# Performance work log

Hardware: AMD Instinct MI355X
Metric: run time of the kernel (lower is better)

The kernel has to match this reference:

```python
import jax, jax.numpy as jnp
import numpy as np

N = 65536
IN_FEAT = 512
OUT_FEAT = 512
K = 16


def setup_inputs() -> dict:
    key = jax.random.key(0)
    k_feat, k_wt, k_wp, k_idx = jax.random.split(key, 4)
    feat = jax.random.normal(k_feat, (N, IN_FEAT), dtype=jnp.float32)
    # nn.Linear(in, out, bias=False): y = x @ W.T with W [out, in].
    # We store W as [in, out] so y = x @ W (same math, transposed layout).
    scale = 1.0 / np.sqrt(IN_FEAT)
    W_theta = jax.random.uniform(k_wt, (IN_FEAT, OUT_FEAT), dtype=jnp.float32, minval=-scale, maxval=scale)
    W_phi = jax.random.uniform(k_wp, (IN_FEAT, OUT_FEAT), dtype=jnp.float32, minval=-scale, maxval=scale)
    src_ind = jax.random.randint(k_idx, (N, K), 0, N, dtype=jnp.int64)
    return {"k": K, "src_ind": src_ind, "feat": feat, "W_theta": W_theta, "W_phi": W_phi}


def reference(k, src_ind, feat, W_theta, W_phi):
    # Dense projections (cuBLAS-friendly part)
    h_theta = feat @ W_theta            # [N, out]
    h_phi = feat @ W_phi                # [N, out]
    h_src = h_theta                     # message contribution from source node
    h_dst = h_phi - h_theta             # per-destination additive term
    # fused_edgeconv_op: result[i] = max_{j in 0..k} (h_src[src_ind[i, j]] + h_dst[i]).
    # h_dst[i] is constant over neighbors, so max commutes with the add:
    neigh = h_src[src_ind[:, :k]]       # [N, k, out] irregular gather
    result = jnp.max(neigh, axis=1) + h_dst  # [N, out]
    return result
```

## Files before the change

kernel.cpp:

```cpp
#include <hip/hip_runtime.h>
#include <hip/hip_bf16.h>
#include <stdint.h>


typedef __bf16 bf16x8 __attribute__((ext_vector_type(8)));
typedef float f32x4 __attribute__((ext_vector_type(4)));

__device__ __forceinline__ unsigned short f2bf(float x) {
    unsigned u = __float_as_uint(x);
    unsigned r = u + 0x7fffu + ((u >> 16) & 1u);
    return (unsigned short)(r >> 16);
}
__device__ __forceinline__ float bf2f(unsigned short b) {
    return __uint_as_float(((unsigned)b) << 16);
}

__device__ __forceinline__ void async_ld16(const void* g, void* l) {
    __builtin_amdgcn_global_load_lds(
        (const __attribute__((address_space(1))) unsigned int*)g,
        (__attribute__((address_space(3))) unsigned int*)l,
        16, 0, 0);
}

__global__ void k_convert_feat(const float* __restrict__ feat,
                               unsigned short* __restrict__ featb) {
    int i = (blockIdx.x * 256 + threadIdx.x) * 4;
    float4 f = *(const float4*)(feat + i);
    ushort4 o;
    o.x = f2bf(f.x); o.y = f2bf(f.y); o.z = f2bf(f.z); o.w = f2bf(f.w);
    *(ushort4*)(featb + i) = o;
}

__global__ void k_prep_w(const float* __restrict__ Wth,
                         const float* __restrict__ Wph,
                         unsigned short* __restrict__ wtc) {
    __shared__ float tile[32][33];
    const int k0 = (blockIdx.x & 15) * 32;
    const int n0 = (blockIdx.x >> 4) * 32;
    const int t  = threadIdx.x;
    const int cc = t & 31;
    const int r0 = t >> 5;
#pragma unroll
    for (int it = 0; it < 4; ++it) {
        const int r  = it * 8 + r0;
        const int gn = n0 + cc;
        float v;
        if (gn < 512) v = Wth[(k0 + r) * 512 + gn];
        else          v = Wph[(k0 + r) * 512 + (gn - 512)] - Wth[(k0 + r) * 512 + (gn - 512)];
        tile[r][cc] = v;
    }
    __syncthreads();
#pragma unroll
    for (int it = 0; it < 4; ++it) {
        const int r2 = t & 31;
        const int c2 = it * 8 + (t >> 5);
        wtc[(size_t)(n0 + c2) * 512 + k0 + r2] = f2bf(tile[r2][c2]);
    }
}

__global__ void k_gemm(const unsigned short* __restrict__ A,
                       const unsigned short* __restrict__ Bt,
                       unsigned short* __restrict__ theta,
                       unsigned short* __restrict__ delta_b,
                       float* __restrict__ delta_f,
                       int dbf)
{
    __shared__ __align__(16) unsigned short As[128 * 32];
    __shared__ __align__(16) unsigned short Bs[128 * 32];

    const int tid  = threadIdx.x;
    const int wave = tid >> 6;
    const int lane = tid & 63;
    const int quad = lane >> 4;
    const int l15  = lane & 15;

    const int b  = blockIdx.x;
    const int mt = (b >> 6) * 8 + (b & 7);
    const int nt = (b >> 3) & 7;
    const int m0 = mt * 128;
    const int n0 = nt * 128;

    const int wm = wave >> 1;
    const int wn = wave & 1;

    f32x4 acc[4][4];
#pragma unroll
    for (int i = 0; i < 4; i++)
#pragma unroll
        for (int j = 0; j < 4; j++) acc[i][j] = (f32x4){0.f, 0.f, 0.f, 0.f};

    const int r0   = (wave * 2 + 0) * 16 + (lane >> 2);
    const int r1   = (wave * 2 + 1) * 16 + (lane >> 2);
    const int koff = (lane & 3) * 8;

    const unsigned short* Ag0 = A  + (size_t)(m0 + r0) * 512 + koff;
    const unsigned short* Ag1 = A  + (size_t)(m0 + r1) * 512 + koff;
    const unsigned short* Bg0 = Bt + (size_t)(n0 + r0) * 512 + koff;
    const unsigned short* Bg1 = Bt + (size_t)(n0 + r1) * 512 + koff;

    unsigned short* lA0 = &As[(wave * 2 + 0) * 512];
    unsigned short* lA1 = &As[(wave * 2 + 1) * 512];
    unsigned short* lB0 = &Bs[(wave * 2 + 0) * 512];
    unsigned short* lB1 = &Bs[(wave * 2 + 1) * 512];

    for (int kt = 0; kt < 16; ++kt) {
        const int kg = kt * 32;
        __syncthreads();
        async_ld16(Ag0 + kg, lA0);
        async_ld16(Ag1 + kg, lA1);
        async_ld16(Bg0 + kg, lB0);
        async_ld16(Bg1 + kg, lB1);
        __syncthreads();

        bf16x8 af[4], bfr[4];
#pragma unroll
        for (int t = 0; t < 4; ++t) {
            const int am = wm * 64 + t * 16 + l15;
            af[t]  = *(const bf16x8*)&As[am * 32 + quad * 8];
            const int bn = wn * 64 + t * 16 + l15;
            bfr[t] = *(const bf16x8*)&Bs[bn * 32 + quad * 8];
        }
#pragma unroll
        for (int i = 0; i < 4; i++)
#pragma unroll
            for (int j = 0; j < 4; j++)
                acc[i][j] = __builtin_amdgcn_mfma_f32_16x16x32_bf16(af[i], bfr[j], acc[i][j], 0, 0, 0);
    }

    const bool is_theta = (n0 < 512);
#pragma unroll
    for (int i = 0; i < 4; i++) {
        const int mrow = m0 + wm * 64 + i * 16 + quad * 4;
#pragma unroll
        for (int j = 0; j < 4; j++) {
            const int ncol = n0 + wn * 64 + j * 16 + l15;
#pragma unroll
            for (int r = 0; r < 4; r++) {
                const float v = acc[i][j][r];
                if (is_theta) {
                    theta[(size_t)(mrow + r) * 512 + ncol] = f2bf(v);
                } else if (dbf) {
                    delta_b[(size_t)(mrow + r) * 512 + (ncol - 512)] = f2bf(v);
                } else {
                    delta_f[(size_t)(mrow + r) * 512 + (ncol - 512)] = v;
                }
            }
        }
    }
}

__global__ void k_gather(const unsigned short* __restrict__ theta,
                         const unsigned short* __restrict__ delta_b,
                         float* out,
                         const int* __restrict__ src,
                         const int* __restrict__ kptr,
                         int srcStride, int dbf)
{
    const int row = (blockIdx.x << 1) + (threadIdx.x >> 7);
    const int c   = (threadIdx.x & 127) << 2;
    const int kk  = *kptr;
    const size_t base = (size_t)row * srcStride;

    float m0 = -INFINITY, m1 = -INFINITY, m2 = -INFINITY, m3 = -INFINITY;
    if (kk == 16) {
#pragma unroll
        for (int k = 0; k < 16; ++k) {
            const int s = src[base + k];
            const uint2 v = *(const uint2*)(theta + (size_t)s * 512 + c);
            m0 = fmaxf(m0, bf2f((unsigned short)(v.x & 0xffffu)));
            m1 = fmaxf(m1, bf2f((unsigned short)(v.x >> 16)));
            m2 = fmaxf(m2, bf2f((unsigned short)(v.y & 0xffffu)));
            m3 = fmaxf(m3, bf2f((unsigned short)(v.y >> 16)));
        }
    } else {
        for (int k = 0; k < kk; ++k) {
            const int s = src[base + k];
            const uint2 v = *(const uint2*)(theta + (size_t)s * 512 + c);
            m0 = fmaxf(m0, bf2f((unsigned short)(v.x & 0xffffu)));
            m1 = fmaxf(m1, bf2f((unsigned short)(v.x >> 16)));
            m2 = fmaxf(m2, bf2f((unsigned short)(v.y & 0xffffu)));
            m3 = fmaxf(m3, bf2f((unsigned short)(v.y >> 16)));
        }
    }

    float d0, d1, d2, d3;
    if (dbf) {
        const uint2 dv = *(const uint2*)(delta_b + (size_t)row * 512 + c);
        d0 = bf2f((unsigned short)(dv.x & 0xffffu));
        d1 = bf2f((unsigned short)(dv.x >> 16));
        d2 = bf2f((unsigned short)(dv.y & 0xffffu));
        d3 = bf2f((unsigned short)(dv.y >> 16));
    } else {
        const float4 dv = *(const float4*)(out + (size_t)row * 512 + c);
        d0 = dv.x; d1 = dv.y; d2 = dv.z; d3 = dv.w;
    }
    float4 o;
    o.x = m0 + d0; o.y = m1 + d1; o.z = m2 + d2; o.w = m3 + d3;
    *(float4*)(out + (size_t)row * 512 + c) = o;
}

extern "C" void kernel_launch(void* const* d_in, const int* in_sizes, int n_in,
                              void* d_out, int out_size, void* d_ws, size_t ws_size,
                              hipStream_t stream) {
    const int*   kptr = (const int*)d_in[0];
    const int*   src  = (const int*)d_in[1];
    const float* feat = (const float*)d_in[2];
    const float* Wth  = (const float*)d_in[3];
    const float* Wph  = (const float*)d_in[4];
    float* out = (float*)d_out;

    const int N = in_sizes[2] / 512;
    const int srcStride = in_sizes[1] / N;

    unsigned short* featb   = (unsigned short*)d_ws;
    unsigned short* wtc     = (unsigned short*)((char*)d_ws + (size_t)64 * 1024 * 1024);
    unsigned short* table   = (unsigned short*)((char*)d_ws + (size_t)65 * 1024 * 1024);
    unsigned short* delta_b = (unsigned short*)((char*)d_ws + (size_t)129 * 1024 * 1024);
    const int dbf = (ws_size >= (size_t)194 * 1024 * 1024) ? 1 : 0;

    k_convert_feat<<<(N * 512) / 1024, 256, 0, stream>>>(feat, featb);
    k_prep_w<<<512, 256, 0, stream>>>(Wth, Wph, wtc);
    k_gemm<<<(N / 128) * 8, 256, 0, stream>>>(featb, wtc, table, delta_b, out, dbf);
    k_gather<<<N / 2, 256, 0, stream>>>(table, delta_b, out, src, kptr, srcStride, dbf);
}
```

Baseline: 475.8 us.

## Slice theta table into 32-column slabs and gather per-slab with XCD-aware scheduling

```diff
diff --git a/kernel.cpp b/kernel.cpp
--- a/kernel.cpp
+++ b/kernel.cpp
@@ -10,9 +10,6 @@
     unsigned u = __float_as_uint(x);
     unsigned r = u + 0x7fffu + ((u >> 16) & 1u);
     return (unsigned short)(r >> 16);
-}
-__device__ __forceinline__ float bf2f(unsigned short b) {
-    return __uint_as_float(((unsigned)b) << 16);
 }
 
 __device__ __forceinline__ void async_ld16(const void* g, void* l) {
@@ -25,7 +22,7 @@
 __global__ void k_convert_feat(const float* __restrict__ feat,
                                unsigned short* __restrict__ featb) {
     int i = (blockIdx.x * 256 + threadIdx.x) * 4;
-    float4 f = *(const float4*)(feat + i);
+    f32x4 f = __builtin_nontemporal_load((const f32x4*)(feat + i));
     ushort4 o;
     o.x = f2bf(f.x); o.y = f2bf(f.y); o.z = f2bf(f.z); o.w = f2bf(f.w);
     *(ushort4*)(featb + i) = o;
@@ -61,9 +58,8 @@
 __global__ void k_gemm(const unsigned short* __restrict__ A,
                        const unsigned short* __restrict__ Bt,
                        unsigned short* __restrict__ theta,
-                       unsigned short* __restrict__ delta_b,
                        float* __restrict__ delta_f,
-                       int dbf)
+                       size_t slabStride)
 {
     __shared__ __align__(16) unsigned short As[128 * 32];
     __shared__ __align__(16) unsigned short Bs[128 * 32];
@@ -138,9 +134,8 @@
             for (int r = 0; r < 4; r++) {
                 const float v = acc[i][j][r];
                 if (is_theta) {
-                    theta[(size_t)(mrow + r) * 512 + ncol] = f2bf(v);
-                } else if (dbf) {
-                    delta_b[(size_t)(mrow + r) * 512 + (ncol - 512)] = f2bf(v);
+                    theta[(size_t)(ncol >> 5) * slabStride
+                          + (size_t)(mrow + r) * 32 + (ncol & 31)] = f2bf(v);
                 } else {
                     delta_f[(size_t)(mrow + r) * 512 + (ncol - 512)] = v;
                 }
@@ -150,53 +145,75 @@
 }
 
 __global__ void k_gather(const unsigned short* __restrict__ theta,
-                         const unsigned short* __restrict__ delta_b,
                          float* out,
                          const int* __restrict__ src,
                          const int* __restrict__ kptr,
-                         int srcStride, int dbf)
+                         int chunksPerSlice, size_t slabStride)
 {
-    const int row = (blockIdx.x << 1) + (threadIdx.x >> 7);
-    const int c   = (threadIdx.x & 127) << 2;
-    const int kk  = *kptr;
-    const size_t base = (size_t)row * srcStride;
-
-    float m0 = -INFINITY, m1 = -INFINITY, m2 = -INFINITY, m3 = -INFINITY;
-    if (kk == 16) {
-#pragma unroll
-        for (int k = 0; k < 16; ++k) {
-            const int s = src[base + k];
-            const uint2 v = *(const uint2*)(theta + (size_t)s * 512 + c);
-            m0 = fmaxf(m0, bf2f((unsigned short)(v.x & 0xffffu)));
-            m1 = fmaxf(m1, bf2f((unsigned short)(v.x >> 16)));
-            m2 = fmaxf(m2, bf2f((unsigned short)(v.y & 0xffffu)));
-            m3 = fmaxf(m3, bf2f((unsigned short)(v.y >> 16)));
+    const int b     = blockIdx.x;
+    const int xcd   = b & 7;
+    const int t2    = b >> 3;
+    const int chunk = t2 % chunksPerSlice;
+    const int phase = t2 / chunksPerSlice;
+    const int slice = phase * 8 + xcd;
+    const int kk    = *kptr;
+
+    const unsigned short* slab = theta + (size_t)slice * slabStride;
+    const int tid = threadIdx.x;
+    const int c8  = (tid & 3) * 8;
+    const int rly = tid >> 2;
+
+#pragma unroll 2
+    for (int pass = 0; pass < 8; ++pass) {
+        const int row = chunk * 512 + pass * 64 + rly;
+
+        float m0 = -INFINITY, m1 = -INFINITY, m2 = -INFINITY, m3 = -INFINITY;
+        float m4 = -INFINITY, m5 = -INFINITY, m6 = -INFINITY, m7 = -INFINITY;
+
+        if (kk == 16) {
+            const int4* sp = (const int4*)(src + (size_t)row * 16);
+            int4 sv[4];
+            sv[0] = sp[0]; sv[1] = sp[1]; sv[2] = sp[2]; sv[3] = sp[3];
+#pragma unroll
+            for (int q = 0; q < 4; ++q) {
+                const int ss[4] = {sv[q].x, sv[q].y, sv[q].z, sv[q].w};
+#pragma unroll
+                for (int j = 0; j < 4; ++j) {
+                    const uint4 v = *(const uint4*)(slab + (size_t)ss[j] * 32 + c8);
+                    m0 = fmaxf(m0, __uint_as_float(v.x << 16));
+                    m1 = fmaxf(m1, __uint_as_float(v.x & 0xffff0000u));
+                    m2 = fmaxf(m2, __uint_as_float(v.y << 16));
+                    m3 = fmaxf(m3, __uint_as_float(v.y & 0xffff0000u));
+                    m4 = fmaxf(m4, __uint_as_float(v.z << 16));
+                    m5 = fmaxf(m5, __uint_as_float(v.z & 0xffff0000u));
+                    m6 = fmaxf(m6, __uint_as_float(v.w << 16));
+                    m7 = fmaxf(m7, __uint_as_float(v.w & 0xffff0000u));
+                }
+            }
+        } else {
+            for (int k = 0; k < kk; ++k) {
+                const int s = src[(size_t)row * 16 + k];
+                const uint4 v = *(const uint4*)(slab + (size_t)s * 32 + c8);
+                m0 = fmaxf(m0, __uint_as_float(v.x << 16));
+                m1 = fmaxf(m1, __uint_as_float(v.x & 0xffff0000u));
+                m2 = fmaxf(m2, __uint_as_float(v.y << 16));
+                m3 = fmaxf(m3, __uint_as_float(v.y & 0xffff0000u));
+                m4 = fmaxf(m4, __uint_as_float(v.z << 16));
+                m5 = fmaxf(m5, __uint_as_float(v.z & 0xffff0000u));
+                m6 = fmaxf(m6, __uint_as_float(v.w << 16));
+                m7 = fmaxf(m7, __uint_as_float(v.w & 0xffff0000u));
+            }
         }
-    } else {
-        for (int k = 0; k < kk; ++k) {
-            const int s = src[base + k];
-            const uint2 v = *(const uint2*)(theta + (size_t)s * 512 + c);
-            m0 = fmaxf(m0, bf2f((unsigned short)(v.x & 0xffffu)));
-            m1 = fmaxf(m1, bf2f((unsigned short)(v.x >> 16)));
-            m2 = fmaxf(m2, bf2f((unsigned short)(v.y & 0xffffu)));
-            m3 = fmaxf(m3, bf2f((unsigned short)(v.y >> 16)));
-        }
-    }
-
-    float d0, d1, d2, d3;
-    if (dbf) {
-        const uint2 dv = *(const uint2*)(delta_b + (size_t)row * 512 + c);
-        d0 = bf2f((unsigned short)(dv.x & 0xffffu));
-        d1 = bf2f((unsigned short)(dv.x >> 16));
-        d2 = bf2f((unsigned short)(dv.y & 0xffffu));
-        d3 = bf2f((unsigned short)(dv.y >> 16));
-    } else {
-        const float4 dv = *(const float4*)(out + (size_t)row * 512 + c);
-        d0 = dv.x; d1 = dv.y; d2 = dv.z; d3 = dv.w;
-    }
-    float4 o;
-    o.x = m0 + d0; o.y = m1 + d1; o.z = m2 + d2; o.w = m3 + d3;
-    *(float4*)(out + (size_t)row * 512 + c) = o;
+
+        float* op = out + (size_t)row * 512 + slice * 32 + c8;
+        const f32x4 d0 = __builtin_nontemporal_load((const f32x4*)op);
+        const f32x4 d1 = __builtin_nontemporal_load((const f32x4*)op + 1);
+        f32x4 o0, o1;
+        o0[0] = m0 + d0[0]; o0[1] = m1 + d0[1]; o0[2] = m2 + d0[2]; o0[3] = m3 + d0[3];
+        o1[0] = m4 + d1[0]; o1[1] = m5 + d1[1]; o1[2] = m6 + d1[2]; o1[3] = m7 + d1[3];
+        __builtin_nontemporal_store(o0, (f32x4*)op);
+        __builtin_nontemporal_store(o1, (f32x4*)op + 1);
+    }
 }
 
 extern "C" void kernel_launch(void* const* d_in, const int* in_sizes, int n_in,
@@ -210,16 +227,17 @@
     float* out = (float*)d_out;
 
     const int N = in_sizes[2] / 512;
-    const int srcStride = in_sizes[1] / N;
-
-    unsigned short* featb   = (unsigned short*)d_ws;
-    unsigned short* wtc     = (unsigned short*)((char*)d_ws + (size_t)64 * 1024 * 1024);
-    unsigned short* table   = (unsigned short*)((char*)d_ws + (size_t)65 * 1024 * 1024);
-    unsigned short* delta_b = (unsigned short*)((char*)d_ws + (size_t)129 * 1024 * 1024);
-    const int dbf = (ws_size >= (size_t)194 * 1024 * 1024) ? 1 : 0;
+    const size_t slabStride = (size_t)N * 32;
+
+    unsigned short* featb = (unsigned short*)d_ws;
+    unsigned short* wtc   = (unsigned short*)((char*)d_ws + (size_t)64 * 1024 * 1024);
+    unsigned short* table = (unsigned short*)((char*)d_ws + (size_t)65 * 1024 * 1024);
+
+    const int chunksPerSlice = N / 512;
 
     k_convert_feat<<<(N * 512) / 1024, 256, 0, stream>>>(feat, featb);
     k_prep_w<<<512, 256, 0, stream>>>(Wth, Wph, wtc);
-    k_gemm<<<(N / 128) * 8, 256, 0, stream>>>(featb, wtc, table, delta_b, out, dbf);
-    k_gather<<<N / 2, 256, 0, stream>>>(table, delta_b, out, src, kptr, srcStride, dbf);
-}
+    k_gemm<<<(N / 128) * 8, 256, 0, stream>>>(featb, wtc, table, out, slabStride);
+    k_gather<<<16 * chunksPerSlice, 256, 0, stream>>>(table, out, src, kptr,
+                                                      chunksPerSlice, slabStride);
+}
```

Measured after the change: 463.2 us. -2.6%, faster.
